# Performance work log

Hardware: AMD Instinct MI355X
Metric: run time of the kernel (lower is better)

The kernel has to match this reference:

```python
import jax, jax.numpy as jnp
import numpy as np

N = 50000
E = 1600000
IN_FEAT = 128
OUT_FEAT = 64
DIM_M = 64          # args.dim_d
D_MAX = 256         # d_max + 1 rows in PE table
OMEGA = 0.1         # args.omega
K_MULT = 1.0        # args.k
N_IDX = 5000


def make_pe():
    pos = np.arange(D_MAX, dtype=np.float64)[:, None]
    i = np.arange(DIM_M, dtype=np.float64)[None, :]
    pe = pos / np.power(10000.0, (i - i % 2) / DIM_M)
    pe[:, 0::2] = np.sin(pe[:, 0::2])
    pe[:, 1::2] = np.cos(pe[:, 1::2])
    return jnp.asarray(pe, dtype=jnp.float32)


def setup_inputs() -> dict:
    key = jax.random.key(0)
    ks = jax.random.split(key, 16)
    x = jax.random.normal(ks[0], (N, IN_FEAT), dtype=jnp.float32)
    edge = jax.random.randint(ks[1], (2, E), 0, N, dtype=jnp.int64)
    degree = jax.random.randint(ks[2], (N, 1), 0, D_MAX, dtype=jnp.int64)
    idx = jax.random.randint(ks[3], (N_IDX,), 0, N, dtype=jnp.int64)
    s = 1.0 / np.sqrt(IN_FEAT)
    W = jax.random.uniform(ks[4], (OUT_FEAT, IN_FEAT), minval=-s, maxval=s)
    b = jax.random.uniform(ks[5], (OUT_FEAT,), minval=-s, maxval=s)
    a = jax.random.normal(ks[6], (1, 2 * OUT_FEAT)) * 0.1   # xavier-ish
    W_gamma = jax.random.uniform(ks[7], (DIM_M, OUT_FEAT))
    W_beta = jax.random.uniform(ks[8], (DIM_M, OUT_FEAT))
    b_gamma = jax.random.uniform(ks[9], (1, OUT_FEAT))
    b_beta = jax.random.uniform(ks[10], (1, OUT_FEAT))
    so = 1.0 / np.sqrt(OUT_FEAT)
    W_add = jax.random.uniform(ks[11], (OUT_FEAT, OUT_FEAT), minval=-so, maxval=so)
    W_rev = jax.random.uniform(ks[12], (OUT_FEAT, OUT_FEAT), minval=-so, maxval=so)
    PE = make_pe()
    return {"x": x, "W": W, "b": b, "a": a, "W_gamma": W_gamma, "W_beta": W_beta,
            "b_gamma": b_gamma, "b_beta": b_beta, "W_add": W_add, "W_rev": W_rev,
            "PE": PE, "edge": edge, "degree": degree, "idx": idx}


def reference(x, W, b, a, W_gamma, W_beta, b_gamma, b_beta, W_add, W_rev, PE, edge, degree, idx):
    lrelu = jax.nn.leaky_relu  # negative_slope=0.01 matches F.leaky_relu default
    h = x @ W.T + b                                   # [N, F] Linear
    h = h * (DIM_M ** 0.5)                            # dataset != 'nba'
    m_dv = PE[degree[:, 0]]                           # [N, dim_M]
    gamma = lrelu(m_dv @ W_gamma + b_gamma)           # [N, F]
    beta = lrelu(m_dv @ W_beta + b_beta)              # [N, F]

    src, dst = edge[0], edge[1]
    deg_f = degree.astype(jnp.float32)                # [N, 1]
    # i = spmm(adj, h) / degree, zeroed where degree == 0
    agg = jax.ops.segment_sum(h[dst], src, num_segments=N)     # adj @ h
    safe_deg = jnp.where(deg_f == 0, 1.0, deg_f)
    i = jnp.where(deg_f == 0, 0.0, agg / safe_deg)

    b_add = (gamma + 1.0) * (i @ W_add.T) + beta
    b_rev = (gamma + 1.0) * (i @ W_rev.T) + beta

    Kthr = jnp.mean(deg_f) * K_MULT
    R = (deg_f < Kthr).astype(jnp.float32)            # [N, 1]

    n_idx = idx.shape[0]
    L_b = (jnp.sum(jnp.linalg.norm((R * b_add)[idx], axis=1)) +
           jnp.sum(jnp.linalg.norm(((1.0 - R) * b_rev)[idx], axis=1))) / n_idx
    L_film = (jnp.sum(jnp.linalg.norm(gamma[idx], axis=1)) +
              jnp.sum(jnp.linalg.norm(beta[idx], axis=1))) / n_idx

    bias = OMEGA * (R * b_add - (1.0 - R) * b_rev)

    # base == 2: GAT-style edge attention.  a @ [h_src; h_dst] = h_src.a1 + h_dst.a2
    s = h @ a[0, :OUT_FEAT]                           # [N]
    t = h @ a[0, OUT_FEAT:]                           # [N]
    edge_e = jnp.exp(-lrelu(s[src] + t[dst]))         # [E]
    e_rowsum = jax.ops.segment_sum(edge_e, src, num_segments=N)[:, None]  # [N,1]
    # dropout in eval mode -> identity
    h_prime = jax.ops.segment_sum(edge_e[:, None] * h[dst], src, num_segments=N)
    h_prime = h_prime + bias
    output = h_prime / (e_rowsum + 1e-5 + 1.0)
    return lrelu(output), L_b, L_film
```

## Files before the change

### kernel.cpp

```cpp
#include <hip/hip_runtime.h>
#include <math.h>

#define N_NODES 50000
#define E_EDGES 1600000
#define IN_F    128
#define OUT_F   64
#define OMEGA   0.1f
#define NIDX    5000
#define NB2     1563
#define CAPG    1536
#define ACH     16384
#define ABLK    98

typedef __attribute__((ext_vector_type(8))) short short8_t;
typedef __attribute__((ext_vector_type(4))) float f32x4;

__device__ __forceinline__ float lrelu(float x) { return x > 0.f ? x : 0.01f * x; }

__device__ __forceinline__ unsigned short f2bf(float f) {
    unsigned u = __float_as_uint(f);
    return (unsigned short)((u + 0x7FFFu + ((u >> 16) & 1u)) >> 16);
}
__device__ __forceinline__ float bf2f(unsigned short v) {
    return __uint_as_float((unsigned)v << 16);
}

__global__ __launch_bounds__(256) void k_node_h(
    const float* __restrict__ x, const float* __restrict__ W,
    const float* __restrict__ b, const float* __restrict__ a,
    unsigned short* __restrict__ h, float* __restrict__ s, float* __restrict__ t)
{
    __shared__ unsigned short xs[64 * 136];
    const int tid = threadIdx.x;
    const int lane = tid & 63, w = tid >> 6;
    const int l15 = lane & 15, l4 = lane >> 4;
    const int row0 = blockIdx.x * 64;

    short8_t bw_[4][4];
    #pragma unroll
    for (int nt = 0; nt < 4; ++nt) {
        #pragma unroll
        for (int ks = 0; ks < 4; ++ks) {
            const float* wp = &W[(nt * 16 + l15) * 128 + ks * 32 + l4 * 8];
            const float4 w0 = *(const float4*)wp;
            const float4 w1 = *(const float4*)(wp + 4);
            short8_t v;
            v[0] = (short)f2bf(w0.x); v[1] = (short)f2bf(w0.y);
            v[2] = (short)f2bf(w0.z); v[3] = (short)f2bf(w0.w);
            v[4] = (short)f2bf(w1.x); v[5] = (short)f2bf(w1.y);
            v[6] = (short)f2bf(w1.z); v[7] = (short)f2bf(w1.w);
            bw_[nt][ks] = v;
        }
    }
    float bcol[4], acol[4], acol2[4];
    #pragma unroll
    for (int nt = 0; nt < 4; ++nt) {
        bcol[nt]  = b[nt * 16 + l15];
        acol[nt]  = a[nt * 16 + l15];
        acol2[nt] = a[64 + nt * 16 + l15];
    }

    for (int f = tid; f < 2048; f += 256) {
        const int row = f >> 5, c4 = f & 31;
        const int rsrc = min(row0 + row, N_NODES - 1);
        const float4 v = *(const float4*)&x[(size_t)rsrc * IN_F + c4 * 4];
        ushort4 u;
        u.x = f2bf(v.x); u.y = f2bf(v.y); u.z = f2bf(v.z); u.w = f2bf(v.w);
        *(ushort4*)&xs[row * 136 + c4 * 4] = u;
    }
    __syncthreads();

    short8_t av[4];
    #pragma unroll
    for (int ks = 0; ks < 4; ++ks)
        av[ks] = *(const short8_t*)&xs[(w * 16 + l15) * 136 + ks * 32 + l4 * 8];

    f32x4 acc[4];
    #pragma unroll
    for (int nt = 0; nt < 4; ++nt) { acc[nt][0]=0.f; acc[nt][1]=0.f; acc[nt][2]=0.f; acc[nt][3]=0.f; }
    #pragma unroll
    for (int nt = 0; nt < 4; ++nt)
        #pragma unroll
        for (int ks = 0; ks < 4; ++ks)
            acc[nt] = __builtin_amdgcn_mfma_f32_16x16x32_bf16(av[ks], bw_[nt][ks], acc[nt], 0, 0, 0);

    float sp[4] = {0.f,0.f,0.f,0.f}, tp[4] = {0.f,0.f,0.f,0.f};
    #pragma unroll
    for (int nt = 0; nt < 4; ++nt) {
        #pragma unroll
        for (int reg = 0; reg < 4; ++reg) {
            const float hv = (acc[nt][reg] + bcol[nt]) * 8.0f;
            const int row = row0 + w * 16 + l4 * 4 + reg;
            if (row < N_NODES) h[(size_t)row * OUT_F + nt * 16 + l15] = f2bf(hv);
            sp[reg] = fmaf(hv, acol[nt],  sp[reg]);
            tp[reg] = fmaf(hv, acol2[nt], tp[reg]);
        }
    }
    #pragma unroll
    for (int reg = 0; reg < 4; ++reg) {
        float sv = sp[reg], tv = tp[reg];
        for (int m = 1; m < 16; m <<= 1) {
            sv += __shfl_xor(sv, m, 64);
            tv += __shfl_xor(tv, m, 64);
        }
        const int row = row0 + w * 16 + l4 * 4 + reg;
        if (l15 == 0 && row < N_NODES) { s[row] = sv; t[row] = tv; }
    }
}

__global__ __launch_bounds__(64) void k_gamma(
    const float* __restrict__ PE, const float* __restrict__ Wg,
    const float* __restrict__ Wb, const float* __restrict__ bg,
    const float* __restrict__ bb, float2* __restrict__ gb2,
    float* __restrict__ gnorm, float* __restrict__ bnorm)
{
    const int d = blockIdx.x, o = threadIdx.x;
    float ga = bg[o], be = bb[o];
    #pragma unroll 8
    for (int k = 0; k < 64; ++k) {
        const float m = PE[d * 64 + k];
        ga = fmaf(m, Wg[k * 64 + o], ga);
        be = fmaf(m, Wb[k * 64 + o], be);
    }
    ga = lrelu(ga); be = lrelu(be);
    gb2[d * 64 + o] = make_float2(ga, be);
    float g2 = ga * ga, b2 = be * be;
    for (int m = 32; m; m >>= 1) {
        g2 += __shfl_down(g2, m, 64);
        b2 += __shfl_down(b2, m, 64);
    }
    if (o == 0) { gnorm[d] = sqrtf(g2); bnorm[d] = sqrtf(b2); }
}

__global__ __launch_bounds__(256) void k_bin(
    const int* __restrict__ edge, const int* __restrict__ degree,
    int* __restrict__ gcursor, unsigned* __restrict__ binned,
    int* __restrict__ degsum)
{
    __shared__ int hist[NB2];
    __shared__ int base[NB2];
    const int tid = threadIdx.x;
    for (int i = tid; i < NB2; i += 256) hist[i] = 0;

    const int gi = blockIdx.x * 256 + tid;
    int dv = 0;
    if (gi < N_NODES) dv += degree[gi];
    if (gi + ABLK * 256 < N_NODES) dv += degree[gi + ABLK * 256];
    for (int off = 32; off; off >>= 1) dv += __shfl_down(dv, off, 64);
    if ((tid & 63) == 0 && dv) atomicAdd(degsum, dv);

    __syncthreads();
    const int e0 = blockIdx.x * ACH;
    const int e1 = min(e0 + ACH, E_EDGES);
    for (int e = e0 + tid; e < e1; e += 256) atomicAdd(&hist[edge[e] >> 5], 1);
    __syncthreads();
    for (int bk = tid; bk < NB2; bk += 256) {
        const int c = hist[bk];
        base[bk] = c ? atomicAdd(&gcursor[bk], c) : 0;
        hist[bk] = 0;
    }
    __syncthreads();
    for (int e = e0 + tid; e < e1; e += 256) {
        const int sv = edge[e];
        const int dvv = edge[E_EDGES + e];
        const int bk = sv >> 5;
        const int pos = base[bk] + atomicAdd(&hist[bk], 1);
        if (pos < CAPG)
            binned[(size_t)bk * CAPG + pos] = ((unsigned)(sv & 31) << 16) | (unsigned)dvv;
    }
}

__global__ __launch_bounds__(256, 4) void k_mega(
    const unsigned* __restrict__ binned, const int* __restrict__ gcursor,
    const unsigned short* __restrict__ h, const float* __restrict__ s,
    const float* __restrict__ t, const int* __restrict__ degree,
    const int* __restrict__ degsum,
    const float* __restrict__ Wadd, const float* __restrict__ Wrev,
    const float2* __restrict__ gb2,
    float* __restrict__ out, float* __restrict__ lb_node)
{
    __shared__ unsigned srt[CAPG];
    __shared__ unsigned short si16[32 * 72];
    __shared__ float hp_l[32 * 68];
    __shared__ float rs_l[32], sv_l[32];
    __shared__ int deg_l[32], cnt[32], curs[32], nbs[33];

    const int tid = threadIdx.x;
    const int lane = tid & 63, w = tid >> 6;
    const int l15 = lane & 15, l4 = lane >> 4;
    const int mat = w >> 1, rt = w & 1;
    const int bkt = blockIdx.x, n0 = bkt * 32;

    const float* __restrict__ Wsel = mat ? Wrev : Wadd;
    short8_t bfr[4][2];
    #pragma unroll
    for (int nt = 0; nt < 4; ++nt) {
        #pragma unroll
        for (int ks = 0; ks < 2; ++ks) {
            const float* wp = &Wsel[(nt * 16 + l15) * 64 + ks * 32 + l4 * 8];
            const float4 w0 = *(const float4*)wp;
            const float4 w1 = *(const float4*)(wp + 4);
            short8_t v;
            v[0] = (short)f2bf(w0.x); v[1] = (short)f2bf(w0.y);
            v[2] = (short)f2bf(w0.z); v[3] = (short)f2bf(w0.w);
            v[4] = (short)f2bf(w1.x); v[5] = (short)f2bf(w1.y);
            v[6] = (short)f2bf(w1.z); v[7] = (short)f2bf(w1.w);
            bfr[nt][ks] = v;
        }
    }

    if (tid < 32) {
        cnt[tid] = 0;
        rs_l[tid] = 0.f;
        const int nd = n0 + tid;
        sv_l[tid]  = (nd < N_NODES) ? s[nd] : 0.f;
        deg_l[tid] = (nd < N_NODES) ? degree[nd] : 0;
    }
    __syncthreads();

    const int cntE = min(gcursor[bkt], CAPG);
    const size_t bb = (size_t)bkt * CAPG;

    for (int j = tid; j < cntE; j += 256)
        atomicAdd(&cnt[binned[bb + j] >> 16], 1);
    __syncthreads();
    if (tid < 32) {
        const int v = cnt[tid];
        int val = v;
        #pragma unroll
        for (int m = 1; m < 32; m <<= 1) {
            const int o = __shfl_up(val, m, 64);
            if (tid >= m) val += o;
        }
        nbs[tid] = val - v;
        curs[tid] = val - v;
        if (tid == 31) nbs[32] = val;
    }
    __syncthreads();
    for (int j = tid; j < cntE; j += 256) {
        const unsigned en = binned[bb + j];
        const int sl = en >> 16;
        const int dvv = en & 0xFFFF;
        const float z = sv_l[sl] + t[dvv];
        const float ee = __expf(-(z > 0.f ? z : 0.01f * z));
        atomicAdd(&rs_l[sl], ee);
        const int p = atomicAdd(&curs[sl], 1);
        srt[p] = (unsigned)dvv | ((unsigned)f2bf(ee) << 16);
    }
    __syncthreads();

    const int g = lane >> 3, ql = lane & 7;
    for (int nl = w; nl < 32; nl += 4) {
        const int rb = nbs[nl], re = nbs[nl + 1];
        float ag[8] = {0.f,0.f,0.f,0.f,0.f,0.f,0.f,0.f};
        float pp[8] = {0.f,0.f,0.f,0.f,0.f,0.f,0.f,0.f};
        #pragma unroll 2
        for (int st = rb; st < re; st += 8) {
            const int j = st + g;
            if (j < re) {
                const unsigned en = srt[j];
                const float ee = bf2f((unsigned short)(en >> 16));
                const int dvv = en & 0xFFFF;
                const short8_t hv = *(const short8_t*)(h + (size_t)dvv * OUT_F + ql * 8);
                #pragma unroll
                for (int c = 0; c < 8; ++c) {
                    const float f = bf2f((unsigned short)hv[c]);
                    ag[c] += f;
                    pp[c] = fmaf(ee, f, pp[c]);
                }
            }
        }
        #pragma unroll
        for (int c = 0; c < 8; ++c) {
            ag[c] += __shfl_xor(ag[c], 8, 64);
            ag[c] += __shfl_xor(ag[c], 16, 64);
            ag[c] += __shfl_xor(ag[c], 32, 64);
            pp[c] += __shfl_xor(pp[c], 8, 64);
            pp[c] += __shfl_xor(pp[c], 16, 64);
            pp[c] += __shfl_xor(pp[c], 32, 64);
        }
        if (lane < 8) {
            const int dg = deg_l[nl];
            const float inv = (dg > 0) ? 1.f / (float)dg : 0.f;
            short8_t iv;
            #pragma unroll
            for (int c = 0; c < 8; ++c) iv[c] = (short)f2bf(ag[c] * inv);
            *(short8_t*)&si16[nl * 72 + lane * 8] = iv;
            float4 h0; h0.x = pp[0]; h0.y = pp[1]; h0.z = pp[2]; h0.w = pp[3];
            float4 h1; h1.x = pp[4]; h1.y = pp[5]; h1.z = pp[6]; h1.w = pp[7];
            *(float4*)&hp_l[nl * 68 + lane * 8]     = h0;
            *(float4*)&hp_l[nl * 68 + lane * 8 + 4] = h1;
        }
    }
    __syncthreads();

    short8_t av[2];
    #pragma unroll
    for (int ks = 0; ks < 2; ++ks)
        av[ks] = *(const short8_t*)&si16[(rt * 16 + l15) * 72 + ks * 32 + l4 * 8];
    f32x4 acc[4];
    #pragma unroll
    for (int nt = 0; nt < 4; ++nt) { acc[nt][0]=0.f; acc[nt][1]=0.f; acc[nt][2]=0.f; acc[nt][3]=0.f; }
    #pragma unroll
    for (int nt = 0; nt < 4; ++nt)
        #pragma unroll
        for (int ks = 0; ks < 2; ++ks)
            acc[nt] = __builtin_amdgcn_mfma_f32_16x16x32_bf16(av[ks], bfr[nt][ks], acc[nt], 0, 0, 0);

    const float kthr = (float)(*degsum) / (float)N_NODES;

    #pragma unroll
    for (int reg = 0; reg < 4; ++reg) {
        const int nl = rt * 16 + l4 * 4 + reg;
        const int node = n0 + nl;
        const bool valid = node < N_NODES;
        const int dg = deg_l[nl];
        const bool rfl = ((float)dg < kthr);
        const bool sel = (rfl == (mat == 0)) && valid;
        const float rdenom = 1.f / (rs_l[nl] + 1e-5f + 1.f);
        const float sgn = (mat == 0) ? OMEGA : -OMEGA;
        float sq = 0.f;
        #pragma unroll
        for (int nt = 0; nt < 4; ++nt) {
            const int o = nt * 16 + l15;
            const float ad = acc[nt][reg];
            const float2 gb = gb2[dg * 64 + o];
            const float bs = fmaf(gb.x + 1.f, ad, gb.y);
            sq = fmaf(bs, bs, sq);
            if (sel) {
                float ov = (hp_l[nl * 68 + o] + sgn * bs) * rdenom;
                ov = ov > 0.f ? ov : 0.01f * ov;
                out[(size_t)node * OUT_F + o] = ov;
            }
        }
        sq += __shfl_xor(sq, 1, 64);
        sq += __shfl_xor(sq, 2, 64);
        sq += __shfl_xor(sq, 4, 64);
        sq += __shfl_xor(sq, 8, 64);
        if (l15 == 0 && sel) lb_node[node] = sqrtf(sq);
    }
}

__global__ __launch_bounds__(1024) void k_loss(
    const int* __restrict__ idx, const int* __restrict__ degree,
    const float* __restrict__ lb_node, const float* __restrict__ gnorm,
    const float* __restrict__ bnorm, float* __restrict__ out)
{
    __shared__ float sb[16], sf[16];
    float lb = 0.f, lf = 0.f;
    for (int i = threadIdx.x; i < NIDX; i += 1024) {
        const int n = idx[i];
        lb += lb_node[n];
        const int dg = degree[n];
        lf += gnorm[dg] + bnorm[dg];
    }
    for (int off = 32; off; off >>= 1) {
        lb += __shfl_down(lb, off, 64);
        lf += __shfl_down(lf, off, 64);
    }
    const int wid = threadIdx.x >> 6;
    if ((threadIdx.x & 63) == 0) { sb[wid] = lb; sf[wid] = lf; }
    __syncthreads();
    if (threadIdx.x == 0) {
        float tb = 0.f, tf = 0.f;
        for (int wv = 0; wv < 16; ++wv) { tb += sb[wv]; tf += sf[wv]; }
        out[(size_t)N_NODES * OUT_F]     = tb / (float)NIDX;
        out[(size_t)N_NODES * OUT_F + 1] = tf / (float)NIDX;
    }
}

extern "C" void kernel_launch(void* const* d_in, const int* in_sizes, int n_in,
                              void* d_out, int out_size, void* d_ws, size_t ws_size,
                              hipStream_t stream)
{
    const float* x    = (const float*)d_in[0];
    const float* W    = (const float*)d_in[1];
    const float* b    = (const float*)d_in[2];
    const float* a    = (const float*)d_in[3];
    const float* Wg   = (const float*)d_in[4];
    const float* Wb   = (const float*)d_in[5];
    const float* bg   = (const float*)d_in[6];
    const float* bb   = (const float*)d_in[7];
    const float* Wadd = (const float*)d_in[8];
    const float* Wrev = (const float*)d_in[9];
    const float* PE   = (const float*)d_in[10];
    const int*  edge   = (const int*)d_in[11];
    const int*  degree = (const int*)d_in[12];
    const int*  idx    = (const int*)d_in[13];
    float* out = (float*)d_out;

    float* ws = (float*)d_ws;
    size_t woff = 0;
    #define ALLOC(nwords) (ws + woff); woff += (((size_t)(nwords)) + 3) & ~(size_t)3;
    const size_t NF = (size_t)N_NODES * OUT_F;
    int*   gcursor = (int*)ALLOC(NB2);
    int*   degsum  = (int*)ALLOC(4);
    unsigned* binned = (unsigned*)ALLOC((size_t)NB2 * CAPG);
    unsigned short* h = (unsigned short*)ALLOC(NF / 2);
    float* s       = ALLOC(N_NODES);
    float* t       = ALLOC(N_NODES);
    float2* gb2    = (float2*)ALLOC(256 * 64 * 2);
    float* gnorm   = ALLOC(256);
    float* bnorm   = ALLOC(256);
    float* lb_node = ALLOC(N_NODES);
    #undef ALLOC

    hipMemsetAsync(d_ws, 0, (NB2 + 8) * sizeof(int), stream);

    k_node_h<<<(N_NODES + 63) / 64, 256, 0, stream>>>(x, W, b, a, h, s, t);
    k_gamma<<<256, 64, 0, stream>>>(PE, Wg, Wb, bg, bb, gb2, gnorm, bnorm);
    k_bin<<<ABLK, 256, 0, stream>>>(edge, degree, gcursor, binned, degsum);
    k_mega<<<NB2, 256, 0, stream>>>(binned, gcursor, h, s, t, degree, degsum,
                                    Wadd, Wrev, gb2, out, lb_node);
    k_loss<<<1, 1024, 0, stream>>>(idx, degree, lb_node, gnorm, bnorm, out);
}
```

Measured before the change: 291.4 us.

## Merge preprocessing kernels into one launch and fold loss reduction into main kernel

Three preprocessing kernels (node linear, gamma/beta table, edge binning) and the degree-sum and idx-multiplicity pass are combined into one kernel, with role chosen by block range. Edge binning now uses one global atomic per edge instead of a shared-memory histogram with per-bucket reservation. The separate loss kernel is removed: the main kernel accumulates loss terms weighted by idx multiplicity through global atomics, and the last block finishes them. The row sum of attention weights now comes from a register reduction instead of shared-memory float atomics. Launch overhead and the serial single-block tail are removed, but there is much more contention on global atomics during binning.

```diff
diff --git a/kernel.cpp b/kernel.cpp
--- a/kernel.cpp
+++ b/kernel.cpp
@@ -9,8 +9,12 @@
 #define NIDX    5000
 #define NB2     1563
 #define CAPG    1536
-#define ACH     16384
-#define ABLK    98
+
+#define GRID_H  782
+#define GRID_G  64
+#define GRID_B  512
+#define GRID_M  20
+#define GRID_A  (GRID_H + GRID_G + GRID_B + GRID_M)
 
 typedef __attribute__((ext_vector_type(8))) short short8_t;
 typedef __attribute__((ext_vector_type(4))) float f32x4;
@@ -25,148 +29,136 @@
     return __uint_as_float((unsigned)v << 16);
 }
 
-__global__ __launch_bounds__(256) void k_node_h(
+__global__ __launch_bounds__(256) void k_pre(
     const float* __restrict__ x, const float* __restrict__ W,
     const float* __restrict__ b, const float* __restrict__ a,
-    unsigned short* __restrict__ h, float* __restrict__ s, float* __restrict__ t)
+    const float* __restrict__ PE, const float* __restrict__ Wg,
+    const float* __restrict__ Wb, const float* __restrict__ bg,
+    const float* __restrict__ bb,
+    const int* __restrict__ edge, const int* __restrict__ degree,
+    const int* __restrict__ idx,
+    unsigned short* __restrict__ h, float* __restrict__ s, float* __restrict__ t,
+    float2* __restrict__ gb2, float* __restrict__ gnorm, float* __restrict__ bnorm,
+    int* __restrict__ gcursor, unsigned* __restrict__ binned,
+    int* __restrict__ degsum, int* __restrict__ mult)
 {
     __shared__ unsigned short xs[64 * 136];
+    const int blk = blockIdx.x;
     const int tid = threadIdx.x;
     const int lane = tid & 63, w = tid >> 6;
-    const int l15 = lane & 15, l4 = lane >> 4;
-    const int row0 = blockIdx.x * 64;
-
-    short8_t bw_[4][4];
-    #pragma unroll
-    for (int nt = 0; nt < 4; ++nt) {
-        #pragma unroll
-        for (int ks = 0; ks < 4; ++ks) {
-            const float* wp = &W[(nt * 16 + l15) * 128 + ks * 32 + l4 * 8];
-            const float4 w0 = *(const float4*)wp;
-            const float4 w1 = *(const float4*)(wp + 4);
-            short8_t v;
-            v[0] = (short)f2bf(w0.x); v[1] = (short)f2bf(w0.y);
-            v[2] = (short)f2bf(w0.z); v[3] = (short)f2bf(w0.w);
-            v[4] = (short)f2bf(w1.x); v[5] = (short)f2bf(w1.y);
-            v[6] = (short)f2bf(w1.z); v[7] = (short)f2bf(w1.w);
-            bw_[nt][ks] = v;
-        }
-    }
-    float bcol[4], acol[4], acol2[4];
-    #pragma unroll
-    for (int nt = 0; nt < 4; ++nt) {
-        bcol[nt]  = b[nt * 16 + l15];
-        acol[nt]  = a[nt * 16 + l15];
-        acol2[nt] = a[64 + nt * 16 + l15];
-    }
-
-    for (int f = tid; f < 2048; f += 256) {
-        const int row = f >> 5, c4 = f & 31;
-        const int rsrc = min(row0 + row, N_NODES - 1);
-        const float4 v = *(const float4*)&x[(size_t)rsrc * IN_F + c4 * 4];
-        ushort4 u;
-        u.x = f2bf(v.x); u.y = f2bf(v.y); u.z = f2bf(v.z); u.w = f2bf(v.w);
-        *(ushort4*)&xs[row * 136 + c4 * 4] = u;
-    }
-    __syncthreads();
-
-    short8_t av[4];
-    #pragma unroll
-    for (int ks = 0; ks < 4; ++ks)
-        av[ks] = *(const short8_t*)&xs[(w * 16 + l15) * 136 + ks * 32 + l4 * 8];
-
-    f32x4 acc[4];
-    #pragma unroll
-    for (int nt = 0; nt < 4; ++nt) { acc[nt][0]=0.f; acc[nt][1]=0.f; acc[nt][2]=0.f; acc[nt][3]=0.f; }
-    #pragma unroll
-    for (int nt = 0; nt < 4; ++nt)
+
+    if (blk < GRID_H) {
+        const int l15 = lane & 15, l4 = lane >> 4;
+        const int row0 = blk * 64;
+
+        short8_t bw_[4][4];
+        #pragma unroll
+        for (int nt = 0; nt < 4; ++nt) {
+            #pragma unroll
+            for (int ks = 0; ks < 4; ++ks) {
+                const float* wp = &W[(nt * 16 + l15) * 128 + ks * 32 + l4 * 8];
+                const float4 w0 = *(const float4*)wp;
+                const float4 w1 = *(const float4*)(wp + 4);
+                short8_t v;
+                v[0] = (short)f2bf(w0.x); v[1] = (short)f2bf(w0.y);
+                v[2] = (short)f2bf(w0.z); v[3] = (short)f2bf(w0.w);
+                v[4] = (short)f2bf(w1.x); v[5] = (short)f2bf(w1.y);
+                v[6] = (short)f2bf(w1.z); v[7] = (short)f2bf(w1.w);
+                bw_[nt][ks] = v;
+            }
+        }
+        float bcol[4], acol[4], acol2[4];
+        #pragma unroll
+        for (int nt = 0; nt < 4; ++nt) {
+            bcol[nt]  = b[nt * 16 + l15];
+            acol[nt]  = a[nt * 16 + l15];
+            acol2[nt] = a[64 + nt * 16 + l15];
+        }
+
+        for (int f = tid; f < 2048; f += 256) {
+            const int row = f >> 5, c4 = f & 31;
+            const int rsrc = min(row0 + row, N_NODES - 1);
+            const float4 v = *(const float4*)&x[(size_t)rsrc * IN_F + c4 * 4];
+            ushort4 u;
+            u.x = f2bf(v.x); u.y = f2bf(v.y); u.z = f2bf(v.z); u.w = f2bf(v.w);
+            *(ushort4*)&xs[row * 136 + c4 * 4] = u;
+        }
+        __syncthreads();
+
+        short8_t av[4];
         #pragma unroll
         for (int ks = 0; ks < 4; ++ks)
-            acc[nt] = __builtin_amdgcn_mfma_f32_16x16x32_bf16(av[ks], bw_[nt][ks], acc[nt], 0, 0, 0);
-
-    float sp[4] = {0.f,0.f,0.f,0.f}, tp[4] = {0.f,0.f,0.f,0.f};
-    #pragma unroll
-    for (int nt = 0; nt < 4; ++nt) {
+            av[ks] = *(const short8_t*)&xs[(w * 16 + l15) * 136 + ks * 32 + l4 * 8];
+
+        f32x4 acc[4];
+        #pragma unroll
+        for (int nt = 0; nt < 4; ++nt) { acc[nt][0]=0.f; acc[nt][1]=0.f; acc[nt][2]=0.f; acc[nt][3]=0.f; }
+        #pragma unroll
+        for (int nt = 0; nt < 4; ++nt)
+            #pragma unroll
+            for (int ks = 0; ks < 4; ++ks)
+                acc[nt] = __builtin_amdgcn_mfma_f32_16x16x32_bf16(av[ks], bw_[nt][ks], acc[nt], 0, 0, 0);
+
+        float sp[4] = {0.f,0.f,0.f,0.f}, tp[4] = {0.f,0.f,0.f,0.f};
+        #pragma unroll
+        for (int nt = 0; nt < 4; ++nt) {
+            #pragma unroll
+            for (int reg = 0; reg < 4; ++reg) {
+                const float hv = (acc[nt][reg] + bcol[nt]) * 8.0f;
+                const int row = row0 + w * 16 + l4 * 4 + reg;
+                if (row < N_NODES) h[(size_t)row * OUT_F + nt * 16 + l15] = f2bf(hv);
+                sp[reg] = fmaf(hv, acol[nt],  sp[reg]);
+                tp[reg] = fmaf(hv, acol2[nt], tp[reg]);
+            }
+        }
         #pragma unroll
         for (int reg = 0; reg < 4; ++reg) {
-            const float hv = (acc[nt][reg] + bcol[nt]) * 8.0f;
+            float sv = sp[reg], tv = tp[reg];
+            for (int m = 1; m < 16; m <<= 1) {
+                sv += __shfl_xor(sv, m, 64);
+                tv += __shfl_xor(tv, m, 64);
+            }
             const int row = row0 + w * 16 + l4 * 4 + reg;
-            if (row < N_NODES) h[(size_t)row * OUT_F + nt * 16 + l15] = f2bf(hv);
-            sp[reg] = fmaf(hv, acol[nt],  sp[reg]);
-            tp[reg] = fmaf(hv, acol2[nt], tp[reg]);
-        }
-    }
-    #pragma unroll
-    for (int reg = 0; reg < 4; ++reg) {
-        float sv = sp[reg], tv = tp[reg];
-        for (int m = 1; m < 16; m <<= 1) {
-            sv += __shfl_xor(sv, m, 64);
-            tv += __shfl_xor(tv, m, 64);
-        }
-        const int row = row0 + w * 16 + l4 * 4 + reg;
-        if (l15 == 0 && row < N_NODES) { s[row] = sv; t[row] = tv; }
-    }
-}
-
-__global__ __launch_bounds__(64) void k_gamma(
-    const float* __restrict__ PE, const float* __restrict__ Wg,
-    const float* __restrict__ Wb, const float* __restrict__ bg,
-    const float* __restrict__ bb, float2* __restrict__ gb2,
-    float* __restrict__ gnorm, float* __restrict__ bnorm)
-{
-    const int d = blockIdx.x, o = threadIdx.x;
-    float ga = bg[o], be = bb[o];
-    #pragma unroll 8
-    for (int k = 0; k < 64; ++k) {
-        const float m = PE[d * 64 + k];
-        ga = fmaf(m, Wg[k * 64 + o], ga);
-        be = fmaf(m, Wb[k * 64 + o], be);
-    }
-    ga = lrelu(ga); be = lrelu(be);
-    gb2[d * 64 + o] = make_float2(ga, be);
-    float g2 = ga * ga, b2 = be * be;
-    for (int m = 32; m; m >>= 1) {
-        g2 += __shfl_down(g2, m, 64);
-        b2 += __shfl_down(b2, m, 64);
-    }
-    if (o == 0) { gnorm[d] = sqrtf(g2); bnorm[d] = sqrtf(b2); }
-}
-
-__global__ __launch_bounds__(256) void k_bin(
-    const int* __restrict__ edge, const int* __restrict__ degree,
-    int* __restrict__ gcursor, unsigned* __restrict__ binned,
-    int* __restrict__ degsum)
-{
-    __shared__ int hist[NB2];
-    __shared__ int base[NB2];
-    const int tid = threadIdx.x;
-    for (int i = tid; i < NB2; i += 256) hist[i] = 0;
-
-    const int gi = blockIdx.x * 256 + tid;
-    int dv = 0;
-    if (gi < N_NODES) dv += degree[gi];
-    if (gi + ABLK * 256 < N_NODES) dv += degree[gi + ABLK * 256];
-    for (int off = 32; off; off >>= 1) dv += __shfl_down(dv, off, 64);
-    if ((tid & 63) == 0 && dv) atomicAdd(degsum, dv);
-
-    __syncthreads();
-    const int e0 = blockIdx.x * ACH;
-    const int e1 = min(e0 + ACH, E_EDGES);
-    for (int e = e0 + tid; e < e1; e += 256) atomicAdd(&hist[edge[e] >> 5], 1);
-    __syncthreads();
-    for (int bk = tid; bk < NB2; bk += 256) {
-        const int c = hist[bk];
-        base[bk] = c ? atomicAdd(&gcursor[bk], c) : 0;
-        hist[bk] = 0;
-    }
-    __syncthreads();
-    for (int e = e0 + tid; e < e1; e += 256) {
-        const int sv = edge[e];
-        const int dvv = edge[E_EDGES + e];
-        const int bk = sv >> 5;
-        const int pos = base[bk] + atomicAdd(&hist[bk], 1);
-        if (pos < CAPG)
-            binned[(size_t)bk * CAPG + pos] = ((unsigned)(sv & 31) << 16) | (unsigned)dvv;
+            if (l15 == 0 && row < N_NODES) { s[row] = sv; t[row] = tv; }
+        }
+    } else if (blk < GRID_H + GRID_G) {
+        const int d = (blk - GRID_H) * 4 + w;
+        const int o = lane;
+        float ga = bg[o], be = bb[o];
+        #pragma unroll 8
+        for (int k = 0; k < 64; ++k) {
+            const float m = PE[d * 64 + k];
+            ga = fmaf(m, Wg[k * 64 + o], ga);
+            be = fmaf(m, Wb[k * 64 + o], be);
+        }
+        ga = lrelu(ga); be = lrelu(be);
+        gb2[d * 64 + o] = make_float2(ga, be);
+        float g2 = ga * ga, b2 = be * be;
+        for (int m2 = 32; m2; m2 >>= 1) {
+            g2 += __shfl_down(g2, m2, 64);
+            b2 += __shfl_down(b2, m2, 64);
+        }
+        if (o == 0) { gnorm[d] = sqrtf(g2); bnorm[d] = sqrtf(b2); }
+    } else if (blk < GRID_H + GRID_G + GRID_B) {
+        const int b0 = blk - GRID_H - GRID_G;
+        for (int e = b0 * 256 + tid; e < E_EDGES; e += GRID_B * 256) {
+            const int sv = edge[e];
+            const int dvv = edge[E_EDGES + e];
+            const int bk = sv >> 5;
+            const int pos = atomicAdd(&gcursor[bk], 1);
+            if (pos < CAPG)
+                binned[(size_t)bk * CAPG + pos] = ((unsigned)(sv & 31) << 16) | (unsigned)dvv;
+        }
+    } else {
+        const int b0 = blk - GRID_H - GRID_G - GRID_B;
+        const int stride = GRID_M * 256;
+        for (int i2 = b0 * 256 + tid; i2 < NIDX; i2 += stride)
+            atomicAdd(&mult[idx[i2]], 1);
+        int dvs = 0;
+        for (int i2 = b0 * 256 + tid; i2 < N_NODES; i2 += stride)
+            dvs += degree[i2];
+        for (int off = 32; off; off >>= 1) dvs += __shfl_down(dvs, off, 64);
+        if (lane == 0 && dvs) atomicAdd(degsum, dvs);
     }
 }
 
@@ -177,7 +169,10 @@
     const int* __restrict__ degsum,
     const float* __restrict__ Wadd, const float* __restrict__ Wrev,
     const float2* __restrict__ gb2,
-    float* __restrict__ out, float* __restrict__ lb_node)
+    const int* __restrict__ mult, const float* __restrict__ gnorm,
+    const float* __restrict__ bnorm,
+    float* __restrict__ out, float* __restrict__ lacc,
+    unsigned* __restrict__ donecnt)
 {
     __shared__ unsigned srt[CAPG];
     __shared__ unsigned short si16[32 * 72];
@@ -211,7 +206,6 @@
 
     if (tid < 32) {
         cnt[tid] = 0;
-        rs_l[tid] = 0.f;
         const int nd = n0 + tid;
         sv_l[tid]  = (nd < N_NODES) ? s[nd] : 0.f;
         deg_l[tid] = (nd < N_NODES) ? degree[nd] : 0;
@@ -243,7 +237,6 @@
         const int dvv = en & 0xFFFF;
         const float z = sv_l[sl] + t[dvv];
         const float ee = __expf(-(z > 0.f ? z : 0.01f * z));
-        atomicAdd(&rs_l[sl], ee);
         const int p = atomicAdd(&curs[sl], 1);
         srt[p] = (unsigned)dvv | ((unsigned)f2bf(ee) << 16);
     }
@@ -254,6 +247,7 @@
         const int rb = nbs[nl], re = nbs[nl + 1];
         float ag[8] = {0.f,0.f,0.f,0.f,0.f,0.f,0.f,0.f};
         float pp[8] = {0.f,0.f,0.f,0.f,0.f,0.f,0.f,0.f};
+        float er = 0.f;
         #pragma unroll 2
         for (int st = rb; st < re; st += 8) {
             const int j = st + g;
@@ -262,6 +256,7 @@
                 const float ee = bf2f((unsigned short)(en >> 16));
                 const int dvv = en & 0xFFFF;
                 const short8_t hv = *(const short8_t*)(h + (size_t)dvv * OUT_F + ql * 8);
+                er += ee;
                 #pragma unroll
                 for (int c = 0; c < 8; ++c) {
                     const float f = bf2f((unsigned short)hv[c]);
@@ -279,6 +274,10 @@
             pp[c] += __shfl_xor(pp[c], 16, 64);
             pp[c] += __shfl_xor(pp[c], 32, 64);
         }
+        er += __shfl_xor(er, 8, 64);
+        er += __shfl_xor(er, 16, 64);
+        er += __shfl_xor(er, 32, 64);
+        if (lane == 0) rs_l[nl] = er;
         if (lane < 8) {
             const int dg = deg_l[nl];
             const float inv = (dg > 0) ? 1.f / (float)dg : 0.f;
@@ -309,6 +308,7 @@
 
     const float kthr = (float)(*degsum) / (float)N_NODES;
 
+    float lbacc = 0.f, lfacc = 0.f;
     #pragma unroll
     for (int reg = 0; reg < 4; ++reg) {
         const int nl = rt * 16 + l4 * 4 + reg;
@@ -337,35 +337,32 @@
         sq += __shfl_xor(sq, 2, 64);
         sq += __shfl_xor(sq, 4, 64);
         sq += __shfl_xor(sq, 8, 64);
-        if (l15 == 0 && sel) lb_node[node] = sqrtf(sq);
-    }
-}
-
-__global__ __launch_bounds__(1024) void k_loss(
-    const int* __restrict__ idx, const int* __restrict__ degree,
-    const float* __restrict__ lb_node, const float* __restrict__ gnorm,
-    const float* __restrict__ bnorm, float* __restrict__ out)
-{
-    __shared__ float sb[16], sf[16];
-    float lb = 0.f, lf = 0.f;
-    for (int i = threadIdx.x; i < NIDX; i += 1024) {
-        const int n = idx[i];
-        lb += lb_node[n];
-        const int dg = degree[n];
-        lf += gnorm[dg] + bnorm[dg];
-    }
-    for (int off = 32; off; off >>= 1) {
-        lb += __shfl_down(lb, off, 64);
-        lf += __shfl_down(lf, off, 64);
-    }
-    const int wid = threadIdx.x >> 6;
-    if ((threadIdx.x & 63) == 0) { sb[wid] = lb; sf[wid] = lf; }
-    __syncthreads();
-    if (threadIdx.x == 0) {
-        float tb = 0.f, tf = 0.f;
-        for (int wv = 0; wv < 16; ++wv) { tb += sb[wv]; tf += sf[wv]; }
-        out[(size_t)N_NODES * OUT_F]     = tb / (float)NIDX;
-        out[(size_t)N_NODES * OUT_F + 1] = tf / (float)NIDX;
+        if (l15 == 0 && sel) {
+            const int mlt = mult[node];
+            if (mlt) {
+                lbacc += (float)mlt * sqrtf(sq);
+                lfacc += (float)mlt * (gnorm[dg] + bnorm[dg]);
+            }
+        }
+    }
+    lbacc += __shfl_xor(lbacc, 16, 64);
+    lbacc += __shfl_xor(lbacc, 32, 64);
+    lfacc += __shfl_xor(lfacc, 16, 64);
+    lfacc += __shfl_xor(lfacc, 32, 64);
+    if (lane == 0 && (lbacc != 0.f || lfacc != 0.f)) {
+        atomicAdd(&lacc[0], lbacc);
+        atomicAdd(&lacc[1], lfacc);
+    }
+    __syncthreads();
+    if (tid == 0) {
+        __threadfence();
+        const unsigned prev = atomicAdd(donecnt, 1u);
+        if (prev == (unsigned)gridDim.x - 1) {
+            const float tb = atomicAdd(&lacc[0], 0.f);
+            const float tf = atomicAdd(&lacc[1], 0.f);
+            out[(size_t)N_NODES * OUT_F]     = tb / (float)NIDX;
+            out[(size_t)N_NODES * OUT_F + 1] = tf / (float)NIDX;
+        }
     }
 }
 
@@ -395,6 +392,10 @@
     const size_t NF = (size_t)N_NODES * OUT_F;
     int*   gcursor = (int*)ALLOC(NB2);
     int*   degsum  = (int*)ALLOC(4);
+    float* lacc    = ALLOC(4);
+    unsigned* donecnt = (unsigned*)ALLOC(4);
+    int*   mult    = (int*)ALLOC(N_NODES);
+    const size_t zero_words = woff;
     unsigned* binned = (unsigned*)ALLOC((size_t)NB2 * CAPG);
     unsigned short* h = (unsigned short*)ALLOC(NF / 2);
     float* s       = ALLOC(N_NODES);
@@ -402,15 +403,15 @@
     float2* gb2    = (float2*)ALLOC(256 * 64 * 2);
     float* gnorm   = ALLOC(256);
     float* bnorm   = ALLOC(256);
-    float* lb_node = ALLOC(N_NODES);
     #undef ALLOC
 
-    hipMemsetAsync(d_ws, 0, (NB2 + 8) * sizeof(int), stream);
-
-    k_node_h<<<(N_NODES + 63) / 64, 256, 0, stream>>>(x, W, b, a, h, s, t);
-    k_gamma<<<256, 64, 0, stream>>>(PE, Wg, Wb, bg, bb, gb2, gnorm, bnorm);
-    k_bin<<<ABLK, 256, 0, stream>>>(edge, degree, gcursor, binned, degsum);
+    hipMemsetAsync(d_ws, 0, zero_words * sizeof(float), stream);
+
+    k_pre<<<GRID_A, 256, 0, stream>>>(x, W, b, a, PE, Wg, Wb, bg, bb,
+                                      edge, degree, idx,
+                                      h, s, t, gb2, gnorm, bnorm,
+                                      gcursor, binned, degsum, mult);
     k_mega<<<NB2, 256, 0, stream>>>(binned, gcursor, h, s, t, degree, degsum,
-                                    Wadd, Wrev, gb2, out, lb_node);
-    k_loss<<<1, 1024, 0, stream>>>(idx, degree, lb_node, gnorm, bnorm, out);
+                                    Wadd, Wrev, gb2, mult, gnorm, bnorm,
+                                    out, lacc, donecnt);
 }
```

After: 516.6 us. 77.3% more time.
